# Performance work log

Hardware: AMD Instinct MI355X
Metric: run time of the kernel (lower is better)

The kernel has to match this reference:

```python
import jax, jax.numpy as jnp
import numpy as np

D = 512      # embed_dim
H = 8        # num_heads
B = 32       # number of graphs
L = 512      # max graph size (padded length)
DEG = 8      # avg out-degree
NUM_GIN = 3  # StructureExtractor num_layers


def setup_inputs() -> dict:
    key = jax.random.key(0)
    ks = jax.random.split(key, 24)

    # ragged graph sizes 256..504, ptr is the CSR boundary vector
    sizes = 256 + 8 * np.arange(B)
    ptr_np = np.concatenate([[0], np.cumsum(sizes)]).astype(np.int64)
    N = int(ptr_np[-1])  # 12160 total nodes

    rng = np.random.RandomState(0)
    node_graph = np.repeat(np.arange(B), sizes)
    offs = ptr_np[node_graph]
    sz = sizes[node_graph]
    # DEG random in-graph neighbors per node
    dst = (rng.random((N, DEG)) * sz[:, None]).astype(np.int64) + offs[:, None]
    src = np.repeat(np.arange(N, dtype=np.int64), DEG)
    edge_index = jnp.asarray(np.stack([src, dst.ravel()]), dtype=jnp.int64)

    # DAG reachability mask: True = masked. Keep key 0 open so no row is fully -inf.
    md = rng.random((B, L, L)) > 0.5
    md[:, :, 0] = False
    mask_dag_ = jnp.asarray(md)

    def lin(k, fan_in, fan_out):
        return jax.random.normal(k, (fan_in, fan_out), jnp.float32) / np.sqrt(fan_in)

    inp = {
        "x": jax.random.normal(ks[0], (N, D), jnp.float32),
        "edge_index": edge_index,
        "mask_dag_": mask_dag_,
        "ptr": jnp.asarray(ptr_np),
        # GIN layers: MLP(Linear(D,D) -> ReLU -> Linear(D,D)) per layer
        "gin_w1": jnp.stack([lin(ks[1 + i], D, D) for i in range(NUM_GIN)]),
        "gin_b1": jnp.zeros((NUM_GIN, D), jnp.float32),
        "gin_w2": jnp.stack([lin(ks[4 + i], D, D) for i in range(NUM_GIN)]),
        "gin_b2": jnp.zeros((NUM_GIN, D), jnp.float32),
        "bn_gamma": jnp.ones((D,), jnp.float32),
        "bn_beta": jnp.zeros((D,), jnp.float32),
        "se_out_w": lin(ks[7], D, D),
        "se_out_b": jnp.zeros((D,), jnp.float32),
        "qk_w": lin(ks[8], D, 2 * D),
        "qk_b": jnp.zeros((2 * D,), jnp.float32),
        "v_w": lin(ks[9], D, D),
        "v_b": jnp.zeros((D,), jnp.float32),
        "out_w": lin(ks[10], D, D),
        "out_b": jnp.zeros((D,), jnp.float32),
    }
    return inp


def reference(x, edge_index, mask_dag_, ptr,
              gin_w1, gin_b1, gin_w2, gin_b2,
              bn_gamma, bn_beta, se_out_w, se_out_b,
              qk_w, qk_b, v_w, v_b, out_w, out_b):
    N = x.shape[0]
    nb = ptr.shape[0] - 1
    Lm = mask_dag_.shape[1]
    hd = D // H
    scale = hd ** -0.5

    # v = to_v(x)
    v = x @ v_w + v_b

    # StructureExtractor: 3 GIN layers (eps=0) + BatchNorm (batch stats) + Linear
    src, dst = edge_index[0], edge_index[1]
    h = x
    for i in range(NUM_GIN):
        agg = jax.ops.segment_sum(h[src], dst, num_segments=N)
        z = h + agg                                  # (1+eps)*x + sum neighbors, eps=0
        z = jax.nn.relu(z @ gin_w1[i] + gin_b1[i]) @ gin_w2[i] + gin_b2[i]
        h = jax.nn.relu(z)
    mean = h.mean(axis=0)
    var = h.var(axis=0)
    h = (h - mean) / jnp.sqrt(var + 1e-5) * bn_gamma + bn_beta
    x_struct = h @ se_out_w + se_out_b

    # qk = to_qk(x_struct).chunk(2): k = first half, q = second half (original order)
    qk = x_struct @ qk_w + qk_b
    k_flat, q_flat = jnp.split(qk, 2, axis=-1)

    # pad ragged batch to [B, L, D]
    node_ar = jnp.arange(N)
    bi = jnp.searchsorted(ptr, node_ar, side='right') - 1   # graph id per node
    pos = node_ar - ptr[bi]                                 # in-graph position
    sizes = ptr[1:] - ptr[:-1]

    def pad(t):
        return jnp.zeros((nb, Lm, t.shape[-1]), t.dtype).at[bi, pos].set(t)

    def heads(t):  # [B, L, D] -> [B, H, L, hd]
        return t.reshape(nb, Lm, H, hd).transpose(0, 2, 1, 3)

    q = heads(pad(q_flat))
    k = heads(pad(k_flat))
    vp = heads(pad(v))

    dots = jnp.einsum('bhid,bhjd->bhij', q, k) * scale
    pad_mask = jnp.arange(Lm)[None, :] >= sizes[:, None]     # True = padded key
    dots = jnp.where(pad_mask[:, None, None, :], -jnp.inf, dots)
    dots = jnp.where(mask_dag_[:, None, :, :], -jnp.inf, dots)
    attn = jax.nn.softmax(dots, axis=-1)

    out = jnp.einsum('bhij,bhjd->bhid', attn, vp)            # [B, H, L, hd]
    out = out.transpose(0, 2, 1, 3).reshape(nb, Lm, D)[bi, pos]  # unpad -> [N, D]
    return out @ out_w + out_b
```

## Files before the change

### kernel.cpp

```cpp
#include <hip/hip_runtime.h>
#include <hip/hip_bf16.h>
#include <cstdint>
#include <cstddef>

#define D 512
#define NHEAD 8
#define LMAX 512
#define NGIN 3

typedef unsigned short u16;
typedef unsigned long long u64;
typedef __attribute__((ext_vector_type(8))) short short8;
typedef __attribute__((ext_vector_type(8))) unsigned short ushort8;
typedef __attribute__((ext_vector_type(4))) unsigned short us4;
typedef __attribute__((ext_vector_type(4))) float f32x4;

static __device__ inline u16 f2bf(float f){
    union { float f; uint32_t u; } c; c.f = f;
    uint32_t r = (c.u + 0x7fffu + ((c.u >> 16) & 1u)) >> 16;
    return (u16)r;
}
static __device__ inline u16 tbf(float f){
    union { float f; uint32_t u; } c; c.f = f;
    return (u16)(c.u >> 16);
}
static __device__ inline float bf2f(u16 h){
    union { uint32_t u; float f; } c; c.u = ((uint32_t)h) << 16; return c.f;
}

#define GLOAD_LDS16(SRC, DST) \
    __builtin_amdgcn_global_load_lds( \
        (const __attribute__((address_space(1))) void*)(SRC), \
        (__attribute__((address_space(3))) void*)(DST), 16, 0, 0)

__global__ __launch_bounds__(256) void probe_mega(const int* __restrict__ ptr_raw,
        const unsigned char* __restrict__ mask_raw, int* __restrict__ flags,
        int* __restrict__ deg, int* __restrict__ cursor,
        float* __restrict__ sums, float* __restrict__ zbias, int N){
    int i = blockIdx.x*256 + threadIdx.x;
    if (i < N){ deg[i] = 0; cursor[i] = 0; }
    if (i < 1024){ sums[i] = 0.f; zbias[i] = 0.f; }
    if (blockIdx.x == 0 && threadIdx.x == 0){
        flags[0] = (ptr_raw[1] == 0) ? 1 : 0;
        int cntOdd = 0, cnt4 = 0;
        for (int k = 1; k < 2048; k += 2) cntOdd += (mask_raw[k] != 0);
        for (int k = 4; k < 2048; k += 8) cnt4   += (mask_raw[k] != 0);
        flags[1] = (cntOdd > 64) ? 1 : ((cnt4 > 16) ? 4 : 8);
    }
}

__global__ __launch_bounds__(256) void mega_prologue(
        const float* __restrict__ v_w, const float* __restrict__ gin_w1,
        const float* __restrict__ gin_w2, const float* __restrict__ se_w,
        const float* __restrict__ out_w, const float* __restrict__ qk_w,
        u16* __restrict__ wtsh, u16* __restrict__ wtsl,
        const unsigned char* __restrict__ mask_raw, u64* __restrict__ mbits,
        const float* __restrict__ x, u16* __restrict__ Xh, u16* __restrict__ Xl,
        u16* __restrict__ sewh, u16* __restrict__ sewl,
        const int* __restrict__ ptr_raw, int* __restrict__ ptr32,
        const int* __restrict__ ei_raw, int* __restrict__ deg,
        const int* __restrict__ flags,
        int Nnodes, int E, int B, int Mn64){
    int z = blockIdx.z;
    int bid = blockIdx.y*32 + blockIdx.x;
    int tid = threadIdx.x;
    if (z <= 9){
        int Nout = (z == 9) ? 1024 : 512;
        if (z < 9 && blockIdx.x >= 16) return;
        const size_t SLOT = 262144;
        const float* W; int slot;
        switch (z){
            case 0: W = v_w; slot = 0; break;
            case 1: W = gin_w1;          slot = 1; break;
            case 2: W = gin_w2;          slot = 2; break;
            case 3: W = gin_w1 + 262144; slot = 3; break;
            case 4: W = gin_w2 + 262144; slot = 4; break;
            case 5: W = gin_w1 + 524288; slot = 5; break;
            case 6: W = gin_w2 + 524288; slot = 6; break;
            case 7: W = se_w;  slot = 7; break;
            case 8: W = out_w; slot = 10; break;
            default: W = qk_w; slot = 8; break;
        }
        u16* Wh = wtsh + SLOT*slot;
        u16* Wl = wtsl + SLOT*slot;
        __shared__ float T[32][33];
        int nb = blockIdx.x*32, kb = blockIdx.y*32;
        int ln = tid & 31, lk = tid >> 5;
        #pragma unroll
        for (int i = 0; i < 4; i++)
            T[lk + 8*i][ln] = W[(size_t)(kb + lk + 8*i)*Nout + nb + ln];
        __syncthreads();
        #pragma unroll
        for (int i = 0; i < 4; i++){
            float val = T[ln][lk + 8*i];
            u16 h = tbf(val);
            size_t idx = (size_t)(nb + lk + 8*i)*512 + kb + ln;
            Wh[idx] = h;
            Wl[idx] = tbf(val - bf2f(h));
        }
    } else if (z == 10){
        int idx = bid*256 + tid;
        if (idx >= Mn64) return;
        int w = flags[1];
        size_t ebase = (size_t)(idx >> 3) * 512 + (size_t)(idx & 7) * 64;
        u64 bits = 0;
        if (w == 1){
            const u64* p8 = (const u64*)(mask_raw + ebase);
            #pragma unroll
            for (int g = 0; g < 8; g++){
                u64 v = p8[g];
                #pragma unroll
                for (int by = 0; by < 8; by++)
                    if ((v >> (by*8)) & 0xffull) bits |= 1ull << (g*8 + by);
            }
        } else {
            for (int j = 0; j < 64; j++)
                if (mask_raw[(ebase + j) * (size_t)w]) bits |= 1ull << j;
        }
        mbits[idx] = bits;
    } else if (z == 11){
        int total4 = Nnodes*D/4;
        for (int i = bid*256 + tid; i < total4; i += 131072){
            float4 v = *(const float4*)(x + (size_t)i*4);
            float fv[4] = {v.x, v.y, v.z, v.w};
            us4 h4, l4;
            #pragma unroll
            for (int j = 0; j < 4; j++){
                u16 hh = tbf(fv[j]);
                h4[j] = hh;
                l4[j] = tbf(fv[j] - bf2f(hh));
            }
            *(us4*)(Xh + (size_t)i*4) = h4;
            *(us4*)(Xl + (size_t)i*4) = l4;
        }
    } else if (z == 12){
        int i = bid*256 + tid;
        if (i >= D*D/4) return;
        float4 v = *(const float4*)(se_w + (size_t)i*4);
        float fv[4] = {v.x, v.y, v.z, v.w};
        us4 h4, l4;
        #pragma unroll
        for (int j = 0; j < 4; j++){
            u16 hh = tbf(fv[j]);
            h4[j] = hh;
            l4[j] = tbf(fv[j] - bf2f(hh));
        }
        *(us4*)(sewh + (size_t)i*4) = h4;
        *(us4*)(sewl + (size_t)i*4) = l4;
    } else if (z == 13){
        if (bid == 0 && tid <= B)
            ptr32[tid] = flags[0] ? ptr_raw[2*tid] : ptr_raw[tid];
    } else {
        int e = bid*256 + tid;
        if (e < E){
            int d = flags[0] ? ei_raw[2*(E + e)] : ei_raw[E + e];
            if ((unsigned)d < (unsigned)Nnodes) atomicAdd(&deg[d], 1);
        }
    }
}

__global__ __launch_bounds__(1024) void scanA(const int* __restrict__ deg,
        int* __restrict__ offs, int* __restrict__ totals, int n){
    __shared__ int wsum[16];
    int ch = blockIdx.x;
    int tid = threadIdx.x, lane = tid & 63, wv = tid >> 6;
    int i = ch*1024 + tid;
    int val = (i < n) ? deg[i] : 0;
    int s = val;
    #pragma unroll
    for (int off = 1; off < 64; off <<= 1){
        int t = __shfl_up(s, off);
        if (lane >= off) s += t;
    }
    if (lane == 63) wsum[wv] = s;
    __syncthreads();
    if (wv == 0){
        int t = (lane < 16) ? wsum[lane] : 0;
        #pragma unroll
        for (int off = 1; off < 16; off <<= 1){
            int u = __shfl_up(t, off);
            if (lane >= off) t += u;
        }
        if (lane < 16) wsum[lane] = t;
    }
    __syncthreads();
    int wbase = wv ? wsum[wv-1] : 0;
    if (i < n) offs[i+1] = wbase + s;
    if (tid == 1023) totals[ch] = wsum[15];
    if (ch == 0 && tid == 0) offs[0] = 0;
}

__global__ void scanB(int* __restrict__ totals, int nch){
    int lane = threadIdx.x;
    int v = (lane < nch) ? totals[lane] : 0;
    int s = v;
    #pragma unroll
    for (int off = 1; off < 64; off <<= 1){
        int t = __shfl_up(s, off);
        if (lane >= off) s += t;
    }
    if (lane < nch) totals[lane] = s - v;
}

__global__ void scanC(int* __restrict__ offs, const int* __restrict__ totals, int n){
    int idx = blockIdx.x*256 + threadIdx.x + 1;
    if (idx <= n) offs[idx] += totals[(idx-1) >> 10];
}

__global__ void fill_kernel(const int* __restrict__ ei_raw, const int* __restrict__ offs,
                            int* __restrict__ cursor, int* __restrict__ in_src,
                            const int* __restrict__ flags, int E, int N){
    int e = blockIdx.x*256 + threadIdx.x;
    if (e < E){
        int d = flags[0] ? ei_raw[2*(E + e)] : ei_raw[E + e];
        if ((unsigned)d < (unsigned)N){
            int slot = atomicAdd(&cursor[d], 1);
            in_src[offs[d] + slot] = flags[0] ? ei_raw[2*e] : ei_raw[e];
        }
    }
}

__global__ __launch_bounds__(256) void gather_kernel(const u16* __restrict__ hh,
        const u16* __restrict__ hl,
        const int* __restrict__ offs, const int* __restrict__ in_src,
        u16* __restrict__ oh, u16* __restrict__ ol, int N){
    int node = blockIdx.x*2 + (threadIdx.x >> 7);
    if (node >= N) return;
    int t = threadIdx.x & 127;
    size_t rb = (size_t)node*D + t*4;
    us4 vh = *(const us4*)(hh + rb);
    us4 vl = *(const us4*)(hl + rb);
    float a[4];
    #pragma unroll
    for (int j = 0; j < 4; j++) a[j] = bf2f(vh[j]) + bf2f(vl[j]);
    int s = offs[node], e = offs[node+1];
    for (int i = s; i < e; i++){
        size_t sb = (size_t)in_src[i]*D + t*4;
        us4 nh = *(const us4*)(hh + sb);
        us4 nl = *(const us4*)(hl + sb);
        #pragma unroll
        for (int j = 0; j < 4; j++) a[j] += bf2f(nh[j]) + bf2f(nl[j]);
    }
    us4 h4, l4;
    #pragma unroll
    for (int j = 0; j < 4; j++){
        u16 hh2 = tbf(a[j]);
        h4[j] = hh2;
        l4[j] = tbf(a[j] - bf2f(hh2));
    }
    *(us4*)(oh + rb) = h4;
    *(us4*)(ol + rb) = l4;
}

__global__ __launch_bounds__(256) void fold_mega(const float* __restrict__ M1,
        const float* __restrict__ sums, const float* __restrict__ gamma,
        const float* __restrict__ beta,
        const float* __restrict__ se_b, const float* __restrict__ qk_w,
        const float* __restrict__ qk_b,
        u16* __restrict__ Wh, u16* __restrict__ Wl, float* __restrict__ bbig, int n){
    float inv_n = 1.f / (float)n;
    if (blockIdx.z == 0){
        __shared__ float T[32][33];
        int nb = blockIdx.x*32, kb = blockIdx.y*32;
        int ln = threadIdx.x & 31, lk = threadIdx.x >> 5;
        #pragma unroll
        for (int i = 0; i < 4; i++){
            int k = kb + lk + 8*i;
            float mean = sums[k] * inv_n;
            float var = sums[512+k] * inv_n - mean*mean;
            float scale = rsqrtf(var + 1e-5f) * gamma[k];
            T[lk + 8*i][ln] = M1[(size_t)k*1024 + nb + ln] * scale;
        }
        __syncthreads();
        #pragma unroll
        for (int i = 0; i < 4; i++){
            float val = T[ln][lk + 8*i];
            u16 h = tbf(val);
            size_t idx = (size_t)(nb + lk + 8*i)*512 + kb + ln;
            Wh[idx] = h;
            Wl[idx] = tbf(val - bf2f(h));
        }
    } else {
        int wv = threadIdx.x >> 6, lane = threadIdx.x & 63;
        if (wv >= 2) return;
        int nidx = (blockIdx.y*32 + blockIdx.x)*2 + wv;
        float acc = 0.f;
        for (int k = lane; k < 512; k += 64){
            float mean = sums[k] * inv_n;
            float var = sums[512+k] * inv_n - mean*mean;
            float scale = rsqrtf(var + 1e-5f) * gamma[k];
            float shift = beta[k] - mean*scale;
            acc += shift*M1[(size_t)k*1024 + nidx] + se_b[k]*qk_w[(size_t)k*1024 + nidx];
        }
        #pragma unroll
        for (int off = 32; off > 0; off >>= 1) acc += __shfl_xor(acc, off);
        if (lane == 0) bbig[nidx] = acc + qk_b[nidx];
    }
}

template<int ACT, int EPI, int TERMS, int STATS>
__global__ __launch_bounds__(256) void gemm_ps(const u16* __restrict__ Ahg,
        const u16* __restrict__ Alg,
        const u16* __restrict__ Wth, const u16* __restrict__ Wtl,
        const float* __restrict__ bias,
        void* __restrict__ C0, void* __restrict__ C1,
        float* __restrict__ stat_sums, int K, int Nout){
    __shared__ __align__(16) u16 Ah[128][64];
    __shared__ __align__(16) u16 Al[TERMS == 3 ? 128 : 1][64];
    __shared__ __align__(16) u16 Bh[64][64];
    __shared__ __align__(16) u16 Bl[64][64];
    int tid = threadIdx.x;
    int gx = gridDim.x;
    int nwg = gx * gridDim.y;
    int orig = blockIdx.x + gx*blockIdx.y;
    int q8 = nwg >> 3, r8 = nwg & 7;
    int xcd = orig & 7, pos = orig >> 3;
    int wg = (xcd < r8 ? xcd*(q8+1) : r8*(q8+1) + (xcd - r8)*q8) + pos;
    int rowBase = (wg / gx) * 128, colBase = (wg % gx) * 64;
    int w = tid >> 6, l = tid & 63, lg = l >> 4, lm = l & 15;
    int wr = w >> 1, wc = w & 1;
    f32x4 acc[4][2] = {};
    const u16* Ahp = Ahg + (size_t)rowBase*K;
    const u16* Alp = (TERMS == 3) ? Alg + (size_t)rowBase*K : nullptr;
    const u16* Wph = Wth + (size_t)colBase*K;
    const u16* Wpl = Wtl + (size_t)colBase*K;
    int srowA[4], scolA[4], srowB[2], scolB[2];
    #pragma unroll
    for (int c = 0; c < 4; c++){
        int slot = c*256 + tid;
        srowA[c] = slot >> 3;
        scolA[c] = ((slot & 7) ^ (srowA[c] & 7)) * 8;
    }
    #pragma unroll
    for (int c = 0; c < 2; c++){
        int slot = c*256 + tid;
        srowB[c] = slot >> 3;
        scolB[c] = ((slot & 7) ^ (srowB[c] & 7)) * 8;
    }
    for (int k0 = 0; k0 < K; k0 += 64){
        #pragma unroll
        for (int c = 0; c < 4; c++){
            int slot = c*256 + tid;
            size_t so = (size_t)srowA[c]*K + k0 + scolA[c];
            GLOAD_LDS16(Ahp + so, &Ah[0][0] + slot*8);
            if (TERMS == 3) GLOAD_LDS16(Alp + so, &Al[0][0] + slot*8);
        }
        #pragma unroll
        for (int c = 0; c < 2; c++){
            int slot = c*256 + tid;
            size_t so = (size_t)srowB[c]*K + k0 + scolB[c];
            GLOAD_LDS16(Wph + so, &Bh[0][0] + slot*8);
            GLOAD_LDS16(Wpl + so, &Bl[0][0] + slot*8);
        }
        __syncthreads();
        #pragma unroll
        for (int ks = 0; ks < 2; ks++){
            int scg = ((ks*4 + lg) ^ (lm & 7)) * 8;
            short8 ah[4], al[4], bh[2], bl[2];
            #pragma unroll
            for (int mf = 0; mf < 4; mf++){
                ah[mf] = *(const short8*)&Ah[wr*64 + mf*16 + lm][scg];
                if (TERMS == 3) al[mf] = *(const short8*)&Al[wr*64 + mf*16 + lm][scg];
            }
            #pragma unroll
            for (int nf = 0; nf < 2; nf++){
                bh[nf] = *(const short8*)&Bh[wc*32 + nf*16 + lm][scg];
                bl[nf] = *(const short8*)&Bl[wc*32 + nf*16 + lm][scg];
            }
            __builtin_amdgcn_s_setprio(1);
            #pragma unroll
            for (int mf = 0; mf < 4; mf++)
                #pragma unroll
                for (int nf = 0; nf < 2; nf++){
                    acc[mf][nf] = __builtin_amdgcn_mfma_f32_16x16x32_bf16(ah[mf], bh[nf], acc[mf][nf], 0, 0, 0);
                    if (TERMS == 3)
                        acc[mf][nf] = __builtin_amdgcn_mfma_f32_16x16x32_bf16(al[mf], bh[nf], acc[mf][nf], 0, 0, 0);
                    acc[mf][nf] = __builtin_amdgcn_mfma_f32_16x16x32_bf16(ah[mf], bl[nf], acc[mf][nf], 0, 0, 0);
                }
            __builtin_amdgcn_s_setprio(0);
        }
        __syncthreads();
    }
    #pragma unroll
    for (int nf = 0; nf < 2; nf++){
        int col = colBase + wc*32 + nf*16 + lm;
        float bv = bias[col];
        float ssum = 0.f, ssq = 0.f;
        #pragma unroll
        for (int mf = 0; mf < 4; mf++){
            int row = rowBase + wr*64 + mf*16 + lg*4;
            #pragma unroll
            for (int j = 0; j < 4; j++){
                float o = acc[mf][nf][j] + bv;
                if (ACT) o = fmaxf(o, 0.f);
                if (STATS){ ssum += o; ssq += o*o; }
                size_t idx = (size_t)(row + j)*Nout + col;
                if (EPI == 0){
                    ((float*)C0)[idx] = o;
                } else if (EPI == 1){
                    u16 hh = tbf(o);
                    ((u16*)C0)[idx] = hh;
                    ((u16*)C1)[idx] = tbf(o - bf2f(hh));
                } else {
                    ((u16*)C0)[idx] = f2bf(o);
                }
            }
        }
        if (STATS){
            ssum += __shfl_xor(ssum, 16); ssum += __shfl_xor(ssum, 32);
            ssq  += __shfl_xor(ssq, 16);  ssq  += __shfl_xor(ssq, 32);
            if (lg == 0){
                atomicAdd(&stat_sums[col], ssum);
                atomicAdd(&stat_sums[512 + col], ssq);
            }
        }
    }
}

#define ATS 72
__global__ __launch_bounds__(512) void attn_mfma_kernel(const u16* __restrict__ qkH,
        const u16* __restrict__ qkL, const u16* __restrict__ vbf,
        const u64* __restrict__ maskbits,
        const int* __restrict__ ptr, u16* __restrict__ oh, int N){
    __shared__ u16 Kh[64][ATS];
    __shared__ u16 Kl[64][ATS];
    __shared__ u16 Vt[64][ATS];
    __shared__ u16 Pl[8][16][ATS];
    int b = blockIdx.z, h = blockIdx.y;
    int base = ptr[b], size = ptr[b+1] - base;
    int q0 = blockIdx.x * 128;
    if (q0 >= size) return;
    int tid = threadIdx.x, w = tid >> 6, l = tid & 63;
    int lg = l >> 4, lm = l & 15;
    short8 qh[2], ql[2];
    {
        int qrow = q0 + w*16 + lm;
        int qr = (qrow < size) ? qrow : 0;
        const u16* qph = qkH + (size_t)(base + qr)*1024 + 512 + h*64;
        const u16* qpl = qkL + (size_t)(base + qr)*1024 + 512 + h*64;
        #pragma unroll
        for (int ks = 0; ks < 2; ks++){
            short8 th = *(const short8*)(qph + ks*32 + lg*8);
            short8 tl = *(const short8*)(qpl + ks*32 + lg*8);
            if (qrow >= size){ th = short8{0,0,0,0,0,0,0,0}; tl = short8{0,0,0,0,0,0,0,0}; }
            qh[ks] = th; ql[ks] = tl;
        }
    }
    f32x4 acco[4] = {};
    float mrow[4], lrow[4];
    #pragma unroll
    for (int j = 0; j < 4; j++){ mrow[j] = -INFINITY; lrow[j] = 0.f; }
    int nt = (size + 63) >> 6;
    for (int t = 0; t < nt; t++){
        int j0 = t*64;
        __syncthreads();
        {
            int jj = tid & 63, db = (tid >> 6)*8;
            int key = j0 + jj;
            bool ok = key < size;
            size_t node = (size_t)(base + (ok ? key : 0));
            const u16* khp = qkH + node*1024 + h*64 + db;
            const u16* klp = qkL + node*1024 + h*64 + db;
            const u16* vp  = vbf + node*512  + h*64 + db;
            ushort8 z = {0,0,0,0,0,0,0,0};
            ushort8 kh0 = ok ? *(const ushort8*)(khp) : z;
            ushort8 kl0 = ok ? *(const ushort8*)(klp) : z;
            ushort8 v0  = ok ? *(const ushort8*)(vp)  : z;
            *(ushort8*)&Kh[jj][db] = kh0;
            *(ushort8*)&Kl[jj][db] = kl0;
            #pragma unroll
            for (int i = 0; i < 8; i++) Vt[db + i][jj] = v0[i];
        }
        __syncthreads();
        f32x4 sc[4] = {};
        __builtin_amdgcn_s_setprio(1);
        #pragma unroll
        for (int nf = 0; nf < 4; nf++)
            #pragma unroll
            for (int ks = 0; ks < 2; ks++){
                short8 kh = *(const short8*)&Kh[nf*16 + lm][ks*32 + lg*8];
                short8 kl = *(const short8*)&Kl[nf*16 + lm][ks*32 + lg*8];
                sc[nf] = __builtin_amdgcn_mfma_f32_16x16x32_bf16(qh[ks], kh, sc[nf], 0, 0, 0);
                sc[nf] = __builtin_amdgcn_mfma_f32_16x16x32_bf16(ql[ks], kh, sc[nf], 0, 0, 0);
                sc[nf] = __builtin_amdgcn_mfma_f32_16x16x32_bf16(qh[ks], kl, sc[nf], 0, 0, 0);
            }
        __builtin_amdgcn_s_setprio(0);
        u64 mb[4];
        #pragma unroll
        for (int j = 0; j < 4; j++)
            mb[j] = maskbits[((size_t)b*LMAX + (q0 + w*16 + lg*4 + j))*8 + t];
        float mx[4], alpha[4];
        #pragma unroll
        for (int j = 0; j < 4; j++){
            float s0 = -INFINITY;
            #pragma unroll
            for (int nf = 0; nf < 4; nf++){
                int key = j0 + nf*16 + lm;
                float s = sc[nf][j] * 0.125f;
                bool msk = (key >= size) || ((mb[j] >> (nf*16 + lm)) & 1);
                s = msk ? -INFINITY : s;
                sc[nf][j] = s;
                s0 = fmaxf(s0, s);
            }
            #pragma unroll
            for (int off = 1; off < 16; off <<= 1) s0 = fmaxf(s0, __shfl_xor(s0, off));
            mx[j] = s0;
        }
        #pragma unroll
        for (int j = 0; j < 4; j++){
            if (mx[j] == -INFINITY){ alpha[j] = 1.f; }
            else {
                float mn = fmaxf(mrow[j], mx[j]);
                alpha[j] = __expf(mrow[j] - mn);
                mrow[j] = mn;
            }
        }
        float ps[4] = {0.f, 0.f, 0.f, 0.f};
        #pragma unroll
        for (int nf = 0; nf < 4; nf++)
            #pragma unroll
            for (int j = 0; j < 4; j++){
                float p = (mx[j] == -INFINITY) ? 0.f : __expf(sc[nf][j] - mrow[j]);
                ps[j] += p;
                Pl[w][lg*4 + j][nf*16 + lm] = tbf(p);
            }
        #pragma unroll
        for (int j = 0; j < 4; j++){
            float s = ps[j];
            #pragma unroll
            for (int off = 1; off < 16; off <<= 1) s += __shfl_xor(s, off);
            lrow[j] = lrow[j]*alpha[j] + s;
        }
        #pragma unroll
        for (int df = 0; df < 4; df++)
            #pragma unroll
            for (int j = 0; j < 4; j++) acco[df][j] *= alpha[j];
        __builtin_amdgcn_s_setprio(1);
        #pragma unroll
        for (int ks = 0; ks < 2; ks++){
            short8 pf = *(const short8*)&Pl[w][lm][ks*32 + lg*8];
            #pragma unroll
            for (int df = 0; df < 4; df++){
                short8 vf = *(const short8*)&Vt[df*16 + lm][ks*32 + lg*8];
                acco[df] = __builtin_amdgcn_mfma_f32_16x16x32_bf16(pf, vf, acco[df], 0, 0, 0);
            }
        }
        __builtin_amdgcn_s_setprio(0);
    }
    #pragma unroll
    for (int j = 0; j < 4; j++){
        int r = q0 + w*16 + lg*4 + j;
        if (r < size){
            float inv = 1.f / lrow[j];
            #pragma unroll
            for (int df = 0; df < 4; df++){
                float o = acco[df][j] * inv;
                oh[(size_t)(base + r)*D + h*64 + df*16 + lm] = f2bf(o);
            }
        }
    }
}

extern "C" void kernel_launch(void* const* d_in, const int* in_sizes, int n_in,
                              void* d_out, int out_size, void* d_ws, size_t ws_size,
                              hipStream_t stream){
    const float* x        = (const float*)d_in[0];
    const int*   ei_raw   = (const int*)d_in[1];
    const unsigned char* mask_raw = (const unsigned char*)d_in[2];
    const int*   ptr_raw  = (const int*)d_in[3];
    const float* gin_w1   = (const float*)d_in[4];
    const float* gin_b1   = (const float*)d_in[5];
    const float* gin_w2   = (const float*)d_in[6];
    const float* gin_b2   = (const float*)d_in[7];
    const float* bn_gamma = (const float*)d_in[8];
    const float* bn_beta  = (const float*)d_in[9];
    const float* se_w     = (const float*)d_in[10];
    const float* se_b     = (const float*)d_in[11];
    const float* qk_w     = (const float*)d_in[12];
    const float* qk_b     = (const float*)d_in[13];
    const float* v_w      = (const float*)d_in[14];
    const float* v_b      = (const float*)d_in[15];
    const float* out_w    = (const float*)d_in[16];
    const float* out_b    = (const float*)d_in[17];

    const int N  = in_sizes[0] / D;
    const int E  = in_sizes[1] / 2;
    const int B  = in_sizes[3] - 1;
    const int Mn = in_sizes[2];

    char* ws = (char*)d_ws;
    char* p = ws;
    auto alloc = [&](size_t bytes) -> char* {
        char* q = p; p += (bytes + 255) & ~(size_t)255; return q;
    };
    size_t PLANE = (size_t)N * D * sizeof(u16);
    u16* pairX = (u16*)alloc(2*PLANE);
    u16* pairG = (u16*)alloc(2*PLANE);
    u16* pairT = (u16*)alloc(2*PLANE);
    u16* pairH = (u16*)alloc(2*PLANE);
    u16* v_bf  = (u16*)alloc(PLANE);
    u16* Xh = pairX, *Xl = pairX + (size_t)N*D;
    u16* Gh = pairG, *Gl = pairG + (size_t)N*D;
    u16* Th = pairT, *Tl = pairT + (size_t)N*D;
    u16* Hh = pairH, *Hl = pairH + (size_t)N*D;
    float* sums   = (float*)alloc(1024*sizeof(float));
    int*   flags  = (int*)alloc(16*sizeof(int));
    int*   deg    = (int*)alloc((size_t)N*sizeof(int));
    int*   offs   = (int*)alloc((size_t)(N+1)*sizeof(int));
    int*   cursor = (int*)alloc((size_t)N*sizeof(int));
    int*   in_src = (int*)alloc((size_t)E*sizeof(int));
    int*   ptr32  = (int*)alloc(64*sizeof(int));
    int*   totals = (int*)alloc(64*sizeof(int));
    u64*   mbits  = (u64*)alloc((size_t)(Mn/64)*sizeof(u64));
    u16*   wtsh   = (u16*)alloc((size_t)2883584*sizeof(u16));
    u16*   wtsl   = (u16*)alloc((size_t)2883584*sizeof(u16));
    u16*   sewh   = (u16*)alloc((size_t)D*D*sizeof(u16));
    u16*   sewl   = (u16*)alloc((size_t)D*D*sizeof(u16));
    float* M1     = (float*)alloc((size_t)D*1024*sizeof(float));
    u16*   wbig_h = (u16*)alloc((size_t)1024*D*sizeof(u16));
    u16*   wbig_l = (u16*)alloc((size_t)1024*D*sizeof(u16));
    float* bbig   = (float*)alloc(1024*sizeof(float));
    float* zbias  = (float*)alloc(1024*sizeof(float));
    const size_t SLOT = 262144;
    u16 *wh_v = wtsh, *wl_v = wtsl;
    u16 *wh_g[6], *wl_g[6];
    for (int i = 0; i < 6; i++){ wh_g[i] = wtsh + SLOT*(1+i); wl_g[i] = wtsl + SLOT*(1+i); }
    u16 *wh_qk  = wtsh + SLOT*8,  *wl_qk  = wtsl + SLOT*8;
    u16 *wh_out = wtsh + SLOT*10, *wl_out = wtsl + SLOT*10;

    probe_mega<<<(N + 255)/256, 256, 0, stream>>>(ptr_raw, mask_raw, flags,
        deg, cursor, sums, zbias, N);
    mega_prologue<<<dim3(32,16,15), 256, 0, stream>>>(
        v_w, gin_w1, gin_w2, se_w, out_w, qk_w, wtsh, wtsl,
        mask_raw, mbits, x, Xh, Xl, sewh, sewl,
        ptr_raw, ptr32, ei_raw, deg, flags, N, E, B, Mn/64);
    int nch = (N + 1023)/1024;
    scanA<<<nch, 1024, 0, stream>>>(deg, offs, totals, N);
    scanB<<<1, 64, 0, stream>>>(totals, nch);
    scanC<<<(N + 255)/256, 256, 0, stream>>>(offs, totals, N);
    fill_kernel<<<(E+255)/256, 256, 0, stream>>>(ei_raw, offs, cursor, in_src, flags, E, N);

    gemm_ps<0,0,3,0><<<dim3(16,4), 256, 0, stream>>>(sewh, sewl, wh_qk, wl_qk, zbias, M1, nullptr, nullptr, D, 2*D);

    dim3 g512(8, N/128), g1024(16, N/128);

    gemm_ps<0,2,2,0><<<g512, 256, 0, stream>>>(Xh, nullptr, wh_v, wl_v, v_b, v_bf, nullptr, nullptr, D, D);

    for (int i = 0; i < NGIN; i++){
        const u16* sh = (i == 0) ? Xh : Hh;
        const u16* sl = (i == 0) ? Xl : Hl;
        gather_kernel<<<(N+1)/2, 256, 0, stream>>>(sh, sl, offs, in_src, Gh, Gl, N);
        gemm_ps<1,1,3,0><<<g512, 256, 0, stream>>>(Gh, Gl, wh_g[2*i], wl_g[2*i], gin_b1 + (size_t)i*D, Th, Tl, nullptr, D, D);
        if (i == NGIN - 1)
            gemm_ps<1,1,3,1><<<g512, 256, 0, stream>>>(Th, Tl, wh_g[2*i+1], wl_g[2*i+1], gin_b2 + (size_t)i*D, Hh, Hl, sums, D, D);
        else
            gemm_ps<1,1,3,0><<<g512, 256, 0, stream>>>(Th, Tl, wh_g[2*i+1], wl_g[2*i+1], gin_b2 + (size_t)i*D, Hh, Hl, nullptr, D, D);
    }

    fold_mega<<<dim3(32,16,2), 256, 0, stream>>>(M1, sums, bn_gamma, bn_beta,
        se_b, qk_w, qk_b, wbig_h, wbig_l, bbig, N);

    gemm_ps<0,1,3,0><<<g1024, 256, 0, stream>>>(Hh, Hl, wbig_h, wbig_l, bbig, pairX, pairG, nullptr, D, 2*D);

    attn_mfma_kernel<<<dim3(LMAX/128, NHEAD, B), 512, 0, stream>>>(pairX, pairG, v_bf, mbits, ptr32, Th, N);

    gemm_ps<0,0,2,0><<<g512, 256, 0, stream>>>(Th, nullptr, wh_out, wl_out, out_b, (float*)d_out, nullptr, nullptr, D, D);
}
```

Baseline: 497.3 us.

## Fold scan fixup into consumers and merge independent GEMMs into one launch

```diff
diff --git a/kernel.cpp b/kernel.cpp
--- a/kernel.cpp
+++ b/kernel.cpp
@@ -202,12 +202,8 @@
     if (lane < nch) totals[lane] = s - v;
 }
 
-__global__ void scanC(int* __restrict__ offs, const int* __restrict__ totals, int n){
-    int idx = blockIdx.x*256 + threadIdx.x + 1;
-    if (idx <= n) offs[idx] += totals[(idx-1) >> 10];
-}
-
 __global__ void fill_kernel(const int* __restrict__ ei_raw, const int* __restrict__ offs,
+                            const int* __restrict__ totals,
                             int* __restrict__ cursor, int* __restrict__ in_src,
                             const int* __restrict__ flags, int E, int N){
     int e = blockIdx.x*256 + threadIdx.x;
@@ -215,14 +211,16 @@
         int d = flags[0] ? ei_raw[2*(E + e)] : ei_raw[E + e];
         if ((unsigned)d < (unsigned)N){
             int slot = atomicAdd(&cursor[d], 1);
-            in_src[offs[d] + slot] = flags[0] ? ei_raw[2*e] : ei_raw[e];
+            int start = offs[d] + (d ? totals[(d-1) >> 10] : 0);
+            in_src[start + slot] = flags[0] ? ei_raw[2*e] : ei_raw[e];
         }
     }
 }
 
 __global__ __launch_bounds__(256) void gather_kernel(const u16* __restrict__ hh,
         const u16* __restrict__ hl,
-        const int* __restrict__ offs, const int* __restrict__ in_src,
+        const int* __restrict__ offs, const int* __restrict__ totals,
+        const int* __restrict__ in_src,
         u16* __restrict__ oh, u16* __restrict__ ol, int N){
     int node = blockIdx.x*2 + (threadIdx.x >> 7);
     if (node >= N) return;
@@ -233,7 +231,8 @@
     float a[4];
     #pragma unroll
     for (int j = 0; j < 4; j++) a[j] = bf2f(vh[j]) + bf2f(vl[j]);
-    int s = offs[node], e = offs[node+1];
+    int s = offs[node] + (node ? totals[(node-1) >> 10] : 0);
+    int e = offs[node+1] + totals[node >> 10];
     for (int i = s; i < e; i++){
         size_t sb = (size_t)in_src[i]*D + t*4;
         us4 nh = *(const us4*)(hh + sb);
@@ -299,24 +298,17 @@
 }
 
 template<int ACT, int EPI, int TERMS, int STATS>
-__global__ __launch_bounds__(256) void gemm_ps(const u16* __restrict__ Ahg,
-        const u16* __restrict__ Alg,
+__device__ __forceinline__ void gemm_body(char* ldsbase,
+        const u16* __restrict__ Ahg, const u16* __restrict__ Alg,
         const u16* __restrict__ Wth, const u16* __restrict__ Wtl,
         const float* __restrict__ bias,
         void* __restrict__ C0, void* __restrict__ C1,
-        float* __restrict__ stat_sums, int K, int Nout){
-    __shared__ __align__(16) u16 Ah[128][64];
-    __shared__ __align__(16) u16 Al[TERMS == 3 ? 128 : 1][64];
-    __shared__ __align__(16) u16 Bh[64][64];
-    __shared__ __align__(16) u16 Bl[64][64];
+        float* __restrict__ stat_sums, int K, int Nout, int rowBase, int colBase){
+    u16 (*Ah)[64] = (u16(*)[64])(ldsbase);
+    u16 (*Al)[64] = (u16(*)[64])(ldsbase + 16384);
+    u16 (*Bh)[64] = (u16(*)[64])(ldsbase + 32768);
+    u16 (*Bl)[64] = (u16(*)[64])(ldsbase + 40960);
     int tid = threadIdx.x;
-    int gx = gridDim.x;
-    int nwg = gx * gridDim.y;
-    int orig = blockIdx.x + gx*blockIdx.y;
-    int q8 = nwg >> 3, r8 = nwg & 7;
-    int xcd = orig & 7, pos = orig >> 3;
-    int wg = (xcd < r8 ? xcd*(q8+1) : r8*(q8+1) + (xcd - r8)*q8) + pos;
-    int rowBase = (wg / gx) * 128, colBase = (wg % gx) * 64;
     int w = tid >> 6, l = tid & 63, lg = l >> 4, lm = l & 15;
     int wr = w >> 1, wc = w & 1;
     f32x4 acc[4][2] = {};
@@ -414,6 +406,56 @@
                 atomicAdd(&stat_sums[512 + col], ssq);
             }
         }
+    }
+}
+
+static __device__ inline void xcd_tile(int gx, int gy, int& rowBase, int& colBase){
+    int nwg = gx * gy;
+    int orig = blockIdx.x + gx*blockIdx.y;
+    int q8 = nwg >> 3, r8 = nwg & 7;
+    int xcd = orig & 7, pos = orig >> 3;
+    int wg = (xcd < r8 ? xcd*(q8+1) : r8*(q8+1) + (xcd - r8)*q8) + pos;
+    rowBase = (wg / gx) * 128;
+    colBase = (wg % gx) * 64;
+}
+
+template<int ACT, int EPI, int TERMS, int STATS>
+__global__ __launch_bounds__(256) void gemm_ps(const u16* __restrict__ Ahg,
+        const u16* __restrict__ Alg,
+        const u16* __restrict__ Wth, const u16* __restrict__ Wtl,
+        const float* __restrict__ bias,
+        void* __restrict__ C0, void* __restrict__ C1,
+        float* __restrict__ stat_sums, int K, int Nout){
+    __shared__ __align__(16) char lds[49152];
+    int rowBase, colBase;
+    xcd_tile(gridDim.x, gridDim.y, rowBase, colBase);
+    gemm_body<ACT,EPI,TERMS,STATS>(lds, Ahg, Alg, Wth, Wtl, bias, C0, C1, stat_sums, K, Nout, rowBase, colBase);
+}
+
+__global__ __launch_bounds__(256) void triple_gemm(
+        const u16* __restrict__ Gh, const u16* __restrict__ Gl,
+        const u16* __restrict__ w1h, const u16* __restrict__ w1l,
+        const float* __restrict__ b1, u16* __restrict__ Th, u16* __restrict__ Tl,
+        const u16* __restrict__ Xh,
+        const u16* __restrict__ wvh, const u16* __restrict__ wvl,
+        const float* __restrict__ vb, u16* __restrict__ vbf,
+        const u16* __restrict__ sewh, const u16* __restrict__ sewl,
+        const u16* __restrict__ wqkh, const u16* __restrict__ wqkl,
+        const float* __restrict__ zbias, float* __restrict__ M1){
+    __shared__ __align__(16) char lds[49152];
+    int z = blockIdx.z;
+    if (z <= 1){
+        int rowBase, colBase;
+        xcd_tile(gridDim.x, gridDim.y, rowBase, colBase);
+        if (z == 0)
+            gemm_body<1,1,3,0>(lds, Gh, Gl, w1h, w1l, b1, Th, Tl, nullptr, 512, 512, rowBase, colBase);
+        else
+            gemm_body<0,2,2,0>(lds, Xh, nullptr, wvh, wvl, vb, vbf, nullptr, nullptr, 512, 512, rowBase, colBase);
+    } else {
+        int orig = blockIdx.x + gridDim.x*blockIdx.y;
+        if (orig >= 64) return;
+        int rowBase = (orig >> 4) * 128, colBase = (orig & 15) * 64;
+        gemm_body<0,0,3,0>(lds, sewh, sewl, wqkh, wqkl, zbias, M1, nullptr, nullptr, 512, 1024, rowBase, colBase);
     }
 }
 
@@ -637,19 +679,19 @@
     int nch = (N + 1023)/1024;
     scanA<<<nch, 1024, 0, stream>>>(deg, offs, totals, N);
     scanB<<<1, 64, 0, stream>>>(totals, nch);
-    scanC<<<(N + 255)/256, 256, 0, stream>>>(offs, totals, N);
-    fill_kernel<<<(E+255)/256, 256, 0, stream>>>(ei_raw, offs, cursor, in_src, flags, E, N);
-
-    gemm_ps<0,0,3,0><<<dim3(16,4), 256, 0, stream>>>(sewh, sewl, wh_qk, wl_qk, zbias, M1, nullptr, nullptr, D, 2*D);
+    fill_kernel<<<(E+255)/256, 256, 0, stream>>>(ei_raw, offs, totals, cursor, in_src, flags, E, N);
 
     dim3 g512(8, N/128), g1024(16, N/128);
 
-    gemm_ps<0,2,2,0><<<g512, 256, 0, stream>>>(Xh, nullptr, wh_v, wl_v, v_b, v_bf, nullptr, nullptr, D, D);
-
-    for (int i = 0; i < NGIN; i++){
-        const u16* sh = (i == 0) ? Xh : Hh;
-        const u16* sl = (i == 0) ? Xl : Hl;
-        gather_kernel<<<(N+1)/2, 256, 0, stream>>>(sh, sl, offs, in_src, Gh, Gl, N);
+    gather_kernel<<<(N+1)/2, 256, 0, stream>>>(Xh, Xl, offs, totals, in_src, Gh, Gl, N);
+    triple_gemm<<<dim3(8, N/128, 3), 256, 0, stream>>>(
+        Gh, Gl, wh_g[0], wl_g[0], gin_b1, Th, Tl,
+        Xh, wh_v, wl_v, v_b, v_bf,
+        sewh, sewl, wh_qk, wl_qk, zbias, M1);
+    gemm_ps<1,1,3,0><<<g512, 256, 0, stream>>>(Th, Tl, wh_g[1], wl_g[1], gin_b2, Hh, Hl, nullptr, D, D);
+
+    for (int i = 1; i < NGIN; i++){
+        gather_kernel<<<(N+1)/2, 256, 0, stream>>>(Hh, Hl, offs, totals, in_src, Gh, Gl, N);
         gemm_ps<1,1,3,0><<<g512, 256, 0, stream>>>(Gh, Gl, wh_g[2*i], wl_g[2*i], gin_b1 + (size_t)i*D, Th, Tl, nullptr, D, D);
         if (i == NGIN - 1)
             gemm_ps<1,1,3,1><<<g512, 256, 0, stream>>>(Th, Tl, wh_g[2*i+1], wl_g[2*i+1], gin_b2 + (size_t)i*D, Hh, Hl, sums, D, D);
```

After: 486.0 us. 1.02x faster.
